# Optimization experiments

Hardware: AMD Instinct MI355X
Metric: run time of the kernel (lower is better)

## Reference

```python
import jax, jax.numpy as jnp
import numpy as np

N, E, F_IN, H, C = 50000, 800000, 50, 128, 121


def setup_inputs() -> dict:
    key = jax.random.key(0)
    ks = jax.random.split(key, 16)
    s = 0.05
    inp = {
        'x': jax.random.normal(ks[0], (N, F_IN), jnp.float32),
        'edge_index': jax.random.randint(ks[1], (2, E), 0, N, jnp.int64),
        'TRAIN': 0,
        'W1': jax.random.normal(ks[2], (F_IN, H), jnp.float32) * s,
        'b1': jnp.zeros((H,), jnp.float32),
        'W2': jax.random.normal(ks[3], (H, H), jnp.float32) * s,
        'b2': jnp.zeros((H,), jnp.float32),
        'W3': jax.random.normal(ks[4], (H, H), jnp.float32) * s,
        'b3': jnp.zeros((H,), jnp.float32),
        'fcW1': jax.random.normal(ks[5], (H, H), jnp.float32) * s,
        'fcb1': jnp.zeros((H,), jnp.float32),
        'fcW2': jax.random.normal(ks[6], (H, H), jnp.float32) * s,
        'fcb2': jnp.zeros((H,), jnp.float32),
        'fcW3': jax.random.normal(ks[7], (H, C), jnp.float32) * s,
        'fcb3': jnp.zeros((C,), jnp.float32),
    }
    return inp


def gcn_conv(x, W, b, src, dst, n):
    # PyG GCNConv: h = x @ W; symmetric norm with self-loops; aggregate at dst.
    h = x @ W
    deg = jax.ops.segment_sum(jnp.ones(src.shape[0], h.dtype), dst, num_segments=n) + 1.0
    dinv = jax.lax.rsqrt(deg)  # deg^{-1/2}, self-loop included
    norm = dinv[src] * dinv[dst]  # [E]
    agg = jax.ops.segment_sum(h[src] * norm[:, None], dst, num_segments=n)
    agg = agg + h * (dinv * dinv)[:, None]  # self-loop contribution
    return agg + b


def reference(x, edge_index, TRAIN, W1, b1, W2, b2, W3, b3, fcW1, fcb1, fcW2, fcb2, fcW3, fcb3):
    src, dst = edge_index[0], edge_index[1]
    n = x.shape[0]
    y = jax.nn.relu(gcn_conv(x, W1, b1, src, dst, n))
    y = jax.nn.relu(gcn_conv(y, W2, b2, src, dst, n))
    y = jax.nn.relu(gcn_conv(y, W3, b3, src, dst, n))
    y = jax.nn.relu(y @ fcW1 + fcb1)
    y = jax.nn.relu(y @ fcW2 + fcb2)
    y = y @ fcW3 + fcb3
    return y
```

## Files before the change

kernel.cpp:

```cpp
#include <hip/hip_runtime.h>

#define SCAN_CHUNK 2048

typedef short s16x8 __attribute__((ext_vector_type(8)));
typedef float f32x4 __attribute__((ext_vector_type(4)));

__device__ inline ushort f2b(float f) {
  uint u = __float_as_uint(f);
  return (ushort)((u + 0x7fffu + ((u >> 16) & 1u)) >> 16);
}
__device__ inline float b2f(uint h) { return __uint_as_float(h << 16); }

__global__ __launch_bounds__(256) void convert_hist_kernel(const void* __restrict__ ei,
                                                           int* __restrict__ src,
                                                           int* __restrict__ dst,
                                                           int* __restrict__ degi, int E) {
  __shared__ int sflag;
  if (threadIdx.x == 0) {
    const int* p32 = (const int*)ei;
    int is64 = 1;
#pragma unroll 4
    for (int i = 1; i < 256; i += 2)
      if (p32[i] != 0) { is64 = 0; break; }
    sflag = is64;
  }
  __syncthreads();
  int e = blockIdx.x * 256 + threadIdx.x;
  if (e >= E) return;
  int s, d;
  if (sflag) {
    const long long* p = (const long long*)ei;
    s = (int)p[e];
    d = (int)p[E + e];
  } else {
    const int* p = (const int*)ei;
    s = p[e];
    d = p[E + e];
  }
  src[e] = s;
  dst[e] = d;
  atomicAdd(&degi[d], 1);
}

__global__ __launch_bounds__(256) void chunk_reduce_kernel(const int* __restrict__ degi,
                                                           int* __restrict__ partials, int N) {
  __shared__ int s[256];
  int base = blockIdx.x * SCAN_CHUNK;
  int sum = 0;
  for (int j = 0; j < 8; ++j) {
    int i = base + threadIdx.x * 8 + j;
    if (i < N) sum += degi[i];
  }
  s[threadIdx.x] = sum;
  __syncthreads();
  for (int ofs = 128; ofs > 0; ofs >>= 1) {
    if ((int)threadIdx.x < ofs) s[threadIdx.x] += s[threadIdx.x + ofs];
    __syncthreads();
  }
  if (threadIdx.x == 0) partials[blockIdx.x] = s[0];
}

__global__ __launch_bounds__(256) void chunk_scan_kernel(int* __restrict__ degi,
                                                         const int* __restrict__ partials,
                                                         int nchunk,
                                                         int* __restrict__ rowptr,
                                                         float* __restrict__ dinv,
                                                         int N, int E) {
  __shared__ int s[256];
  __shared__ int sbase;
  int t = threadIdx.x;
  if (t == 0) {
    int acc = 0;
    for (int c = 0; c < (int)blockIdx.x; ++c) acc += partials[c];
    sbase = acc;
    if (blockIdx.x == 0) rowptr[N] = E;
  }
  int base = blockIdx.x * SCAN_CHUNK;
  int v[8];
  int tsum = 0;
  for (int j = 0; j < 8; ++j) {
    int i = base + t * 8 + j;
    v[j] = (i < N) ? degi[i] : 0;
    tsum += v[j];
  }
  s[t] = tsum;
  __syncthreads();
  for (int ofs = 1; ofs < 256; ofs <<= 1) {
    int add = (t >= ofs) ? s[t - ofs] : 0;
    __syncthreads();
    s[t] += add;
    __syncthreads();
  }
  int run = s[t] - tsum + sbase;
  for (int j = 0; j < 8; ++j) {
    int i = base + t * 8 + j;
    if (i < N) {
      rowptr[i] = run;
      dinv[i] = rsqrtf((float)v[j] + 1.0f);
      degi[i] = 0;
    }
    run += v[j];
  }
}

__global__ __launch_bounds__(256) void scatter_kernel(const int* __restrict__ src,
                                                      const int* __restrict__ dst,
                                                      const int* __restrict__ rowptr,
                                                      const float* __restrict__ dinv,
                                                      int* __restrict__ cnt,
                                                      uint* __restrict__ epack, int E, int N) {
  const int chunk = blockIdx.x & 7;
  const int group = blockIdx.x >> 3;
  const int ngroup = gridDim.x >> 3;
  const int c0 = (int)(((long)chunk * N) >> 3);
  const int c1 = (int)(((long)(chunk + 1) * N) >> 3);
  for (int e = group * 256 + threadIdx.x; e < E; e += ngroup * 256) {
    int d = dst[e];
    if (d < c0 || d >= c1) continue;
    int s = src[e];
    int slot = rowptr[d] + atomicAdd(&cnt[d], 1);
    float nm = dinv[s] * dinv[d];
    epack[slot] = (uint)s | ((uint)f2b(nm) << 16);
  }
}

__global__ __launch_bounds__(256) void prep_all(const float* __restrict__ W1,
                                                const float* __restrict__ W2,
                                                const float* __restrict__ W3,
                                                const float* __restrict__ F1,
                                                const float* __restrict__ F2,
                                                const float* __restrict__ F3,
                                                const float* __restrict__ x,
                                                ushort* __restrict__ W1t, ushort* __restrict__ W2t,
                                                ushort* __restrict__ W3t, ushort* __restrict__ F1t,
                                                ushort* __restrict__ F2t, ushort* __restrict__ F3t,
                                                ushort* __restrict__ xb, int N) {
  int b = blockIdx.x;
  if (b < 384) {
    int wi = b >> 6;
    int i = (b & 63) * 256 + threadIdx.x;
    const float* W;
    ushort* Wt;
    int K, Kp, ncol;
    switch (wi) {
      case 0: W = W1; Wt = W1t; K = 50; Kp = 64; ncol = 128; break;
      case 1: W = W2; Wt = W2t; K = 128; Kp = 128; ncol = 128; break;
      case 2: W = W3; Wt = W3t; K = 128; Kp = 128; ncol = 128; break;
      case 3: W = F1; Wt = F1t; K = 128; Kp = 128; ncol = 128; break;
      case 4: W = F2; Wt = F2t; K = 128; Kp = 128; ncol = 128; break;
      default: W = F3; Wt = F3t; K = 128; Kp = 128; ncol = 121; break;
    }
    if (i >= 128 * Kp) return;
    int c = i / Kp, k = i - c * Kp;
    float w = (k < K && c < ncol) ? W[(size_t)k * ncol + c] : 0.f;
    ushort hi = f2b(w);
    float rem = w - b2f(hi);
    Wt[(size_t)c * Kp + k] = hi;
    Wt[(size_t)128 * Kp + (size_t)c * Kp + k] = f2b(rem);
  } else {
    long i = (long)(b - 384) * 256 + threadIdx.x;
    if (i >= (long)N * 64) return;
    int n = (int)(i >> 6), k = (int)(i & 63);
    xb[i] = (k < 50) ? f2b(x[(size_t)n * 50 + k]) : (ushort)0;
  }
}

template <int KSTEPS, bool BIAS, bool RELU>
__global__ __launch_bounds__(256) void mm_mfma(const ushort* __restrict__ X,
                                               const ushort* __restrict__ Wt,
                                               const float* __restrict__ bias,
                                               ushort* __restrict__ Yb, int N) {
  constexpr int K = KSTEPS * 32;
  const int lane = threadIdx.x & 63;
  const int wid = (blockIdx.x * 256 + threadIdx.x) >> 6;
  const long r0 = (long)wid * 32;
  if (r0 >= N) return;
  const bool v1 = (r0 + 16) < N;
  const int am = lane & 15;
  const int ag = lane >> 4;
  const ushort* __restrict__ wbase = Wt + (size_t)am * K + ag * 8;
  const ushort* __restrict__ x0 = X + (size_t)(r0 + am) * K + ag * 8;

  f32x4 acc[2][8] = {};
  for (int ks = 0; ks < KSTEPS; ++ks) {
    s16x8 a0 = *(const s16x8*)(x0 + ks * 32);
    s16x8 a1 = {};
    if (v1) a1 = *(const s16x8*)(x0 + (size_t)16 * K + ks * 32);
#pragma unroll
    for (int f = 0; f < 8; ++f) {
      const ushort* wp = wbase + (size_t)f * 16 * K + ks * 32;
      s16x8 bh = *(const s16x8*)(wp);
      s16x8 bl = *(const s16x8*)(wp + (size_t)128 * K);
      acc[0][f] = __builtin_amdgcn_mfma_f32_16x16x32_bf16(a0, bh, acc[0][f], 0, 0, 0);
      acc[0][f] = __builtin_amdgcn_mfma_f32_16x16x32_bf16(a0, bl, acc[0][f], 0, 0, 0);
      if (v1) {
        acc[1][f] = __builtin_amdgcn_mfma_f32_16x16x32_bf16(a1, bh, acc[1][f], 0, 0, 0);
        acc[1][f] = __builtin_amdgcn_mfma_f32_16x16x32_bf16(a1, bl, acc[1][f], 0, 0, 0);
      }
    }
  }

  const int dr = (lane >> 4) * 4;
  const int dc = lane & 15;
#pragma unroll
  for (int m = 0; m < 2; ++m) {
    if (m == 1 && !v1) break;
#pragma unroll
    for (int f = 0; f < 8; ++f) {
      int col = f * 16 + dc;
      float bv = BIAS ? bias[col] : 0.f;
#pragma unroll
      for (int r = 0; r < 4; ++r) {
        long row = r0 + m * 16 + dr + r;
        float v = acc[m][f][r] + bv;
        if (RELU) v = fmaxf(v, 0.f);
        Yb[row * 128 + col] = f2b(v);
      }
    }
  }
}

__global__ __launch_bounds__(256) void fc_fused(const ushort* __restrict__ X,
                                                const ushort* __restrict__ F1t,
                                                const ushort* __restrict__ F2t,
                                                const ushort* __restrict__ F3t,
                                                const float* __restrict__ b1,
                                                const float* __restrict__ b2,
                                                const float* __restrict__ b3,
                                                float* __restrict__ out, int N) {
  __shared__ ushort lds[4][32 * 128];
  const int lane = threadIdx.x & 63;
  const int wv = threadIdx.x >> 6;
  const int wid = (blockIdx.x * 256 + threadIdx.x) >> 6;
  const long r0 = (long)wid * 32;
  if (r0 >= N) return;
  const bool v1 = (r0 + 16) < N;
  const int am = lane & 15;
  const int ag = lane >> 4;
  char* my = (char*)lds[wv];

  auto stage = [&](f32x4 acc[2][8], const float* __restrict__ bias) {
#pragma unroll
    for (int m = 0; m < 2; ++m)
#pragma unroll
      for (int f = 0; f < 8; ++f) {
        int col = f * 16 + am;
        float bv = bias[col];
#pragma unroll
        for (int r = 0; r < 4; ++r) {
          int row = m * 16 + ag * 4 + r;
          uint byte = (uint)(row * 256 + col * 2) ^ ((uint)(row & 7) << 4);
          *(ushort*)(my + byte) = f2b(fmaxf(acc[m][f][r] + bv, 0.f));
        }
      }
  };
  auto loadA = [&](int m, int ks) -> s16x8 {
    int row = m * 16 + am;
    uint byte = (uint)(row * 256 + ks * 64 + ag * 16) ^ ((uint)(row & 7) << 4);
    return *(const s16x8*)(my + byte);
  };
  auto layer = [&](f32x4 acc[2][8], const ushort* __restrict__ Wt, bool fromLds,
                   const ushort* __restrict__ x0) {
#pragma unroll
    for (int ks = 0; ks < 4; ++ks) {
      s16x8 a0, a1;
      if (fromLds) {
        a0 = loadA(0, ks);
        a1 = loadA(1, ks);
      } else {
        a0 = *(const s16x8*)(x0 + ks * 32);
        a1 = v1 ? *(const s16x8*)(x0 + (size_t)16 * 128 + ks * 32) : s16x8{};
      }
      const ushort* wb = Wt + (size_t)am * 128 + ag * 8;
#pragma unroll
      for (int f = 0; f < 8; ++f) {
        const ushort* wp = wb + (size_t)f * 16 * 128 + ks * 32;
        s16x8 bh = *(const s16x8*)(wp);
        s16x8 bl = *(const s16x8*)(wp + (size_t)128 * 128);
        acc[0][f] = __builtin_amdgcn_mfma_f32_16x16x32_bf16(a0, bh, acc[0][f], 0, 0, 0);
        acc[0][f] = __builtin_amdgcn_mfma_f32_16x16x32_bf16(a0, bl, acc[0][f], 0, 0, 0);
        acc[1][f] = __builtin_amdgcn_mfma_f32_16x16x32_bf16(a1, bh, acc[1][f], 0, 0, 0);
        acc[1][f] = __builtin_amdgcn_mfma_f32_16x16x32_bf16(a1, bl, acc[1][f], 0, 0, 0);
      }
    }
  };

  const ushort* x0 = X + (size_t)(r0 + am) * 128 + ag * 8;
  f32x4 acc[2][8] = {};
  layer(acc, F1t, false, x0);
  stage(acc, b1);
  f32x4 acc2[2][8] = {};
  layer(acc2, F2t, true, nullptr);
  stage(acc2, b2);
  f32x4 acc3[2][8] = {};
  layer(acc3, F3t, true, nullptr);

#pragma unroll
  for (int m = 0; m < 2; ++m) {
    if (m == 1 && !v1) break;
#pragma unroll
    for (int f = 0; f < 8; ++f) {
      int col = f * 16 + am;
      if (col >= 121) continue;
      float bv = b3[col];
#pragma unroll
      for (int r = 0; r < 4; ++r) {
        long row = r0 + m * 16 + ag * 4 + r;
        if (row < N) out[row * 121 + col] = acc3[m][f][r] + bv;
      }
    }
  }
}

template <int RW, bool ACT>
__global__ __launch_bounds__(256) void agg_kernel(const ushort* __restrict__ Hm,
                                                  const int* __restrict__ rowptr,
                                                  const uint* __restrict__ epack,
                                                  const float* __restrict__ dinv,
                                                  const float* __restrict__ b,
                                                  ushort* __restrict__ Y, int N) {
  int wave = threadIdx.x >> 6;
  int lane = threadIdx.x & 63;
  int n = blockIdx.x * 4 + wave;
  if (n >= N) return;
  int beg = rowptr[n], end = rowptr[n + 1];
  float dn = dinv[n];
  float d2 = dn * dn;
  int i = beg;

  if constexpr (RW == 128) {
    int f = lane * 2;
    float ax = 0.f, ay = 0.f;
    while (i + 8 <= end) {
      uint rec[8];
#pragma unroll
      for (int j = 0; j < 8; ++j) rec[j] = epack[i + j];
      uint v[8];
#pragma unroll
      for (int j = 0; j < 8; ++j)
        v[j] = *(const uint*)&Hm[(size_t)(rec[j] & 0xffffu) * 128 + f];
#pragma unroll
      for (int j = 0; j < 8; ++j) {
        float nm = __uint_as_float(rec[j] & 0xffff0000u);
        ax += b2f(v[j] & 0xffffu) * nm;
        ay += b2f(v[j] >> 16) * nm;
      }
      i += 8;
    }
    if (i + 4 <= end) {
      uint rec[4];
#pragma unroll
      for (int j = 0; j < 4; ++j) rec[j] = epack[i + j];
      uint v[4];
#pragma unroll
      for (int j = 0; j < 4; ++j)
        v[j] = *(const uint*)&Hm[(size_t)(rec[j] & 0xffffu) * 128 + f];
#pragma unroll
      for (int j = 0; j < 4; ++j) {
        float nm = __uint_as_float(rec[j] & 0xffff0000u);
        ax += b2f(v[j] & 0xffffu) * nm;
        ay += b2f(v[j] >> 16) * nm;
      }
      i += 4;
    }
    for (; i < end; ++i) {
      uint rec = epack[i];
      float nm = __uint_as_float(rec & 0xffff0000u);
      uint v = *(const uint*)&Hm[(size_t)(rec & 0xffffu) * 128 + f];
      ax += b2f(v & 0xffffu) * nm;
      ay += b2f(v >> 16) * nm;
    }
    uint sv = *(const uint*)&Hm[(size_t)n * 128 + f];
    ax += b2f(sv & 0xffffu) * d2;
    ay += b2f(sv >> 16) * d2;
    if (ACT) {
      ax = fmaxf(ax + b[f], 0.f);
      ay = fmaxf(ay + b[f + 1], 0.f);
    }
    uint out = (uint)f2b(ax) | ((uint)f2b(ay) << 16);
    *(uint*)&Y[(size_t)n * 128 + f] = out;
  } else {
    int f = lane;
    float ax = 0.f;
    while (i + 8 <= end) {
      uint rec[8];
#pragma unroll
      for (int j = 0; j < 8; ++j) rec[j] = epack[i + j];
      ushort v[8];
#pragma unroll
      for (int j = 0; j < 8; ++j)
        v[j] = Hm[(size_t)(rec[j] & 0xffffu) * 64 + f];
#pragma unroll
      for (int j = 0; j < 8; ++j)
        ax += b2f(v[j]) * __uint_as_float(rec[j] & 0xffff0000u);
      i += 8;
    }
    if (i + 4 <= end) {
      uint rec[4];
#pragma unroll
      for (int j = 0; j < 4; ++j) rec[j] = epack[i + j];
      ushort v[4];
#pragma unroll
      for (int j = 0; j < 4; ++j)
        v[j] = Hm[(size_t)(rec[j] & 0xffffu) * 64 + f];
#pragma unroll
      for (int j = 0; j < 4; ++j)
        ax += b2f(v[j]) * __uint_as_float(rec[j] & 0xffff0000u);
      i += 4;
    }
    for (; i < end; ++i) {
      uint rec = epack[i];
      ax += b2f(Hm[(size_t)(rec & 0xffffu) * 64 + f]) * __uint_as_float(rec & 0xffff0000u);
    }
    ax += b2f(Hm[(size_t)n * 64 + f]) * d2;
    if (ACT) ax = fmaxf(ax + b[f], 0.f);
    Y[(size_t)n * 64 + f] = f2b(ax);
  }
}

extern "C" void kernel_launch(void* const* d_in, const int* in_sizes, int n_in,
                              void* d_out, int out_size, void* d_ws, size_t ws_size,
                              hipStream_t stream) {
  const float* x    = (const float*)d_in[0];
  const void*  ei   = d_in[1];
  const float* W1   = (const float*)d_in[3];
  const float* b1   = (const float*)d_in[4];
  const float* W2   = (const float*)d_in[5];
  const float* b2   = (const float*)d_in[6];
  const float* W3   = (const float*)d_in[7];
  const float* b3   = (const float*)d_in[8];
  const float* fcW1 = (const float*)d_in[9];
  const float* fcb1 = (const float*)d_in[10];
  const float* fcW2 = (const float*)d_in[11];
  const float* fcb2 = (const float*)d_in[12];
  const float* fcW3 = (const float*)d_in[13];
  const float* fcb3 = (const float*)d_in[14];

  const int FIN = 50;
  const int N = in_sizes[0] / FIN;
  const int E = in_sizes[1] / 2;
  const int NCHUNK = (N + SCAN_CHUNK - 1) / SCAN_CHUNK;

  size_t off = 0;
  auto carve = [&](size_t bytes) {
    void* p = (char*)d_ws + off;
    off += (bytes + 255) & ~(size_t)255;
    return p;
  };
  int*    src32    = (int*)carve((size_t)E * 4);
  int*    dst32    = (int*)carve((size_t)E * 4);
  uint*   epack    = (uint*)carve((size_t)E * 4);
  int*    degi     = (int*)carve((size_t)N * 4);
  int*    rowptr   = (int*)carve((size_t)(N + 1) * 4);
  float*  dinv     = (float*)carve((size_t)N * 4);
  int*    partials = (int*)carve((size_t)NCHUNK * 4);
  ushort* W1t      = (ushort*)carve((size_t)2 * 128 * 64 * 2);
  ushort* W2t      = (ushort*)carve((size_t)2 * 128 * 128 * 2);
  ushort* W3t      = (ushort*)carve((size_t)2 * 128 * 128 * 2);
  ushort* F1t      = (ushort*)carve((size_t)2 * 128 * 128 * 2);
  ushort* F2t      = (ushort*)carve((size_t)2 * 128 * 128 * 2);
  ushort* F3t      = (ushort*)carve((size_t)2 * 128 * 128 * 2);
  ushort* xb       = (ushort*)carve((size_t)N * 64 * 2);
  ushort* aggX     = (ushort*)carve((size_t)N * 64 * 2);
  ushort* bufA     = (ushort*)carve((size_t)N * 128 * 2);
  ushort* bufB     = (ushort*)carve((size_t)N * 128 * 2);

  const int gE = (E + 255) / 256;
  const int gMM = (N + 127) / 128;
  const int gAGG = (N + 3) / 4;
  const int gPREP = 384 + (int)(((long)N * 64 + 255) / 256);

  hipMemsetAsync(degi, 0, (size_t)N * 4, stream);
  convert_hist_kernel<<<gE, 256, 0, stream>>>(ei, src32, dst32, degi, E);
  chunk_reduce_kernel<<<NCHUNK, 256, 0, stream>>>(degi, partials, N);
  chunk_scan_kernel<<<NCHUNK, 256, 0, stream>>>(degi, partials, NCHUNK, rowptr, dinv, N, E);
  scatter_kernel<<<1024, 256, 0, stream>>>(src32, dst32, rowptr, dinv, degi, epack, E, N);
  prep_all<<<gPREP, 256, 0, stream>>>(W1, W2, W3, fcW1, fcW2, fcW3, x,
                                      W1t, W2t, W3t, F1t, F2t, F3t, xb, N);

  agg_kernel<64, false><<<gAGG, 256, 0, stream>>>(xb, rowptr, epack, dinv, nullptr, aggX, N);
  mm_mfma<2, true, true><<<gMM, 256, 0, stream>>>(aggX, W1t, b1, bufA, N);
  mm_mfma<4, false, false><<<gMM, 256, 0, stream>>>(bufA, W2t, nullptr, bufB, N);
  agg_kernel<128, true><<<gAGG, 256, 0, stream>>>(bufB, rowptr, epack, dinv, b2, bufA, N);
  mm_mfma<4, false, false><<<gMM, 256, 0, stream>>>(bufA, W3t, nullptr, bufB, N);
  agg_kernel<128, true><<<gAGG, 256, 0, stream>>>(bufB, rowptr, epack, dinv, b3, bufA, N);
  fc_fused<<<gMM, 256, 0, stream>>>(bufA, F1t, F2t, F3t, fcb1, fcb2, fcb3,
                                    (float*)d_out, N);
}
```

Before: 318.3 us.

## Split output columns across four waves per 32-row block in MFMA GEMMs

The dense GEMM and fused FC kernels change from one wave computing 32 rows by all 128 columns to a block of four waves sharing 32 rows, each wave owning 32 output columns. This cuts per-wave accumulator registers from 16 to 4 MFMA tiles, which should raise occupancy and quadruple the grid size. In return, each A tile is loaded redundantly by four waves, and the fused FC kernel needs a shared LDS tile with __syncthreads barriers between layers.

```diff
diff --git a/kernel.cpp b/kernel.cpp
--- a/kernel.cpp
+++ b/kernel.cpp
@@ -172,23 +172,22 @@
                                                ushort* __restrict__ Yb, int N) {
   constexpr int K = KSTEPS * 32;
   const int lane = threadIdx.x & 63;
-  const int wid = (blockIdx.x * 256 + threadIdx.x) >> 6;
-  const long r0 = (long)wid * 32;
+  const int wq = threadIdx.x >> 6;
+  const long r0 = (long)blockIdx.x * 32;
   if (r0 >= N) return;
   const bool v1 = (r0 + 16) < N;
   const int am = lane & 15;
   const int ag = lane >> 4;
-  const ushort* __restrict__ wbase = Wt + (size_t)am * K + ag * 8;
   const ushort* __restrict__ x0 = X + (size_t)(r0 + am) * K + ag * 8;
 
-  f32x4 acc[2][8] = {};
+  f32x4 acc[2][2] = {};
   for (int ks = 0; ks < KSTEPS; ++ks) {
     s16x8 a0 = *(const s16x8*)(x0 + ks * 32);
     s16x8 a1 = {};
     if (v1) a1 = *(const s16x8*)(x0 + (size_t)16 * K + ks * 32);
 #pragma unroll
-    for (int f = 0; f < 8; ++f) {
-      const ushort* wp = wbase + (size_t)f * 16 * K + ks * 32;
+    for (int f = 0; f < 2; ++f) {
+      const ushort* wp = Wt + (size_t)(wq * 32 + f * 16 + am) * K + ag * 8 + ks * 32;
       s16x8 bh = *(const s16x8*)(wp);
       s16x8 bl = *(const s16x8*)(wp + (size_t)128 * K);
       acc[0][f] = __builtin_amdgcn_mfma_f32_16x16x32_bf16(a0, bh, acc[0][f], 0, 0, 0);
@@ -200,14 +199,13 @@
     }
   }
 
-  const int dr = (lane >> 4) * 4;
-  const int dc = lane & 15;
+  const int dr = ag * 4;
 #pragma unroll
   for (int m = 0; m < 2; ++m) {
     if (m == 1 && !v1) break;
 #pragma unroll
-    for (int f = 0; f < 8; ++f) {
-      int col = f * 16 + dc;
+    for (int f = 0; f < 2; ++f) {
+      int col = wq * 32 + f * 16 + am;
       float bv = BIAS ? bias[col] : 0.f;
 #pragma unroll
       for (int r = 0; r < 4; ++r) {
@@ -228,23 +226,22 @@
                                                 const float* __restrict__ b2,
                                                 const float* __restrict__ b3,
                                                 float* __restrict__ out, int N) {
-  __shared__ ushort lds[4][32 * 128];
+  __shared__ ushort lds[32 * 128];
   const int lane = threadIdx.x & 63;
-  const int wv = threadIdx.x >> 6;
-  const int wid = (blockIdx.x * 256 + threadIdx.x) >> 6;
-  const long r0 = (long)wid * 32;
+  const int wq = threadIdx.x >> 6;
+  const long r0 = (long)blockIdx.x * 32;
   if (r0 >= N) return;
   const bool v1 = (r0 + 16) < N;
   const int am = lane & 15;
   const int ag = lane >> 4;
-  char* my = (char*)lds[wv];
-
-  auto stage = [&](f32x4 acc[2][8], const float* __restrict__ bias) {
+  char* my = (char*)lds;
+
+  auto stage = [&](f32x4 acc[2][2], const float* __restrict__ bias) {
 #pragma unroll
     for (int m = 0; m < 2; ++m)
 #pragma unroll
-      for (int f = 0; f < 8; ++f) {
-        int col = f * 16 + am;
+      for (int f = 0; f < 2; ++f) {
+        int col = wq * 32 + f * 16 + am;
         float bv = bias[col];
 #pragma unroll
         for (int r = 0; r < 4; ++r) {
@@ -259,7 +256,7 @@
     uint byte = (uint)(row * 256 + ks * 64 + ag * 16) ^ ((uint)(row & 7) << 4);
     return *(const s16x8*)(my + byte);
   };
-  auto layer = [&](f32x4 acc[2][8], const ushort* __restrict__ Wt, bool fromLds,
+  auto layer = [&](f32x4 acc[2][2], const ushort* __restrict__ Wt, bool fromLds,
                    const ushort* __restrict__ x0) {
 #pragma unroll
     for (int ks = 0; ks < 4; ++ks) {
@@ -271,10 +268,9 @@
         a0 = *(const s16x8*)(x0 + ks * 32);
         a1 = v1 ? *(const s16x8*)(x0 + (size_t)16 * 128 + ks * 32) : s16x8{};
       }
-      const ushort* wb = Wt + (size_t)am * 128 + ag * 8;
-#pragma unroll
-      for (int f = 0; f < 8; ++f) {
-        const ushort* wp = wb + (size_t)f * 16 * 128 + ks * 32;
+#pragma unroll
+      for (int f = 0; f < 2; ++f) {
+        const ushort* wp = Wt + (size_t)(wq * 32 + f * 16 + am) * 128 + ag * 8 + ks * 32;
         s16x8 bh = *(const s16x8*)(wp);
         s16x8 bl = *(const s16x8*)(wp + (size_t)128 * 128);
         acc[0][f] = __builtin_amdgcn_mfma_f32_16x16x32_bf16(a0, bh, acc[0][f], 0, 0, 0);
@@ -286,27 +282,30 @@
   };
 
   const ushort* x0 = X + (size_t)(r0 + am) * 128 + ag * 8;
-  f32x4 acc[2][8] = {};
-  layer(acc, F1t, false, x0);
-  stage(acc, b1);
-  f32x4 acc2[2][8] = {};
-  layer(acc2, F2t, true, nullptr);
-  stage(acc2, b2);
-  f32x4 acc3[2][8] = {};
-  layer(acc3, F3t, true, nullptr);
+  f32x4 a1c[2][2] = {};
+  layer(a1c, F1t, false, x0);
+  stage(a1c, b1);
+  __syncthreads();
+  f32x4 a2c[2][2] = {};
+  layer(a2c, F2t, true, nullptr);
+  __syncthreads();
+  stage(a2c, b2);
+  __syncthreads();
+  f32x4 a3c[2][2] = {};
+  layer(a3c, F3t, true, nullptr);
 
 #pragma unroll
   for (int m = 0; m < 2; ++m) {
     if (m == 1 && !v1) break;
 #pragma unroll
-    for (int f = 0; f < 8; ++f) {
-      int col = f * 16 + am;
+    for (int f = 0; f < 2; ++f) {
+      int col = wq * 32 + f * 16 + am;
       if (col >= 121) continue;
       float bv = b3[col];
 #pragma unroll
       for (int r = 0; r < 4; ++r) {
         long row = r0 + m * 16 + ag * 4 + r;
-        if (row < N) out[row * 121 + col] = acc3[m][f][r] + bv;
+        if (row < N) out[row * 121 + col] = a3c[m][f][r] + bv;
       }
     }
   }
@@ -466,7 +465,7 @@
   ushort* bufB     = (ushort*)carve((size_t)N * 128 * 2);
 
   const int gE = (E + 255) / 256;
-  const int gMM = (N + 127) / 128;
+  const int gMM = (N + 31) / 32;
   const int gAGG = (N + 3) / 4;
   const int gPREP = 384 + (int)(((long)N * 64 + 255) / 256);
 
```

After: 307.2 us. 3.5% less time.
